# Kernel tuning notes

Measured on AMD Instinct MI355X. Metric: run time of the kernel, lower is better.

## Reference

```python
import jax, jax.numpy as jnp
import numpy as np

B, M, N, D, W = 4, 4096, 4096, 128, 128  # batch/heads, rows, cols, head dim, nnz per row


def setup_inputs() -> dict:
    key = jax.random.key(0)
    kq, kk, kv, kc = jax.random.split(key, 4)
    q3d = jax.random.normal(kq, (B, M, D), dtype=jnp.float32)
    k3d = jax.random.normal(kk, (B, N, D), dtype=jnp.float32)
    v3d = jax.random.normal(kv, (B, N, D), dtype=jnp.float32)
    # CSR with uniform W nonzeros per row: row_offsets = arange(M+1)*W implicitly
    column_indices = jnp.sort(
        jax.random.randint(kc, (M, W), 0, N), axis=-1
    ).astype(jnp.int32)
    return {"q3d": q3d, "k3d": k3d, "v3d": v3d, "column_indices": column_indices}


def reference(q3d, k3d, v3d, column_indices):
    # SDDMM: logits[b, i, j] = q[b, i, :] . k[b, col[i, j], :]  (no 1/sqrt(d) scaling,
    # matching the original module which applies none)
    k_gath = k3d[:, column_indices, :]                     # [B, M, W, D]
    logits = jnp.einsum('bmd,bmwd->bmw', q3d, k_gath)      # [B, M, W]
    # Sparse row-wise softmax over the nonzeros of each row
    weights = jax.nn.softmax(logits, axis=-1)              # [B, M, W]
    # SPMM: out[b, i, :] = sum_j weights[b, i, j] * v[b, col[i, j], :]
    v_gath = v3d[:, column_indices, :]                     # [B, M, W, D]
    out = jnp.einsum('bmw,bmwd->bmd', weights, v_gath)     # [B, M, D]
    return out
```

## Files before the change

kernel.cpp:

```cpp
#include <hip/hip_runtime.h>


typedef __attribute__((ext_vector_type(2))) _Float16 half2v;
typedef __attribute__((ext_vector_type(8))) _Float16 half8;

constexpr int Bc = 4, Mc = 4096, Nc = 4096, Dc = 128, Wc = 128;
constexpr size_t KV_ELEMS = (size_t)Bc * Nc * Dc;
constexpr float EPS_SCREEN = 3e-6f;
constexpr float QS = 127.f / 6.f;
constexpr float INV_S = 1.f / (QS * QS);

__global__ __launch_bounds__(256) void cvt_kernel(
    const float* __restrict__ k3d, _Float16* __restrict__ kh,
    unsigned int* __restrict__ ki8)
{
    const size_t i = ((size_t)blockIdx.x * blockDim.x + threadIdx.x) * 8;
    if (i >= KV_ELEMS) return;
    const float4 ka = *reinterpret_cast<const float4*>(k3d + i);
    const float4 kb = *reinterpret_cast<const float4*>(k3d + i + 4);
    half8 hk;
    hk[0]=(_Float16)ka.x; hk[1]=(_Float16)ka.y; hk[2]=(_Float16)ka.z; hk[3]=(_Float16)ka.w;
    hk[4]=(_Float16)kb.x; hk[5]=(_Float16)kb.y; hk[6]=(_Float16)kb.z; hk[7]=(_Float16)kb.w;
    *reinterpret_cast<half8*>(kh + i) = hk;
    float f[8] = {ka.x, ka.y, ka.z, ka.w, kb.x, kb.y, kb.z, kb.w};
    unsigned int w0 = 0, w1 = 0;
    #pragma unroll
    for (int j = 0; j < 4; ++j) {
        int v = __float2int_rn(f[j] * QS);
        v = max(-127, min(127, v));
        w0 |= ((unsigned int)(v & 0xFF)) << (8 * j);
    }
    #pragma unroll
    for (int j = 0; j < 4; ++j) {
        int v = __float2int_rn(f[4 + j] * QS);
        v = max(-127, min(127, v));
        w1 |= ((unsigned int)(v & 0xFF)) << (8 * j);
    }
    *reinterpret_cast<uint2*>(ki8 + i / 4) = make_uint2(w0, w1);
}

__device__ __forceinline__ float dot8_f16(const half8& qv, const half8& kv) {
    const half2v q0 = {qv[0], qv[1]}, q1 = {qv[2], qv[3]},
                 q2 = {qv[4], qv[5]}, q3 = {qv[6], qv[7]};
    const half2v k0 = {kv[0], kv[1]}, k1 = {kv[2], kv[3]},
                 k2 = {kv[4], kv[5]}, k3 = {kv[6], kv[7]};
    float p = __builtin_amdgcn_fdot2(q0, k0, 0.f, false);
    p = __builtin_amdgcn_fdot2(q1, k1, p, false);
    p = __builtin_amdgcn_fdot2(q2, k2, p, false);
    p = __builtin_amdgcn_fdot2(q3, k3, p, false);
    return p;
}

__global__ __launch_bounds__(64) void sparse_attn_r10(
    const float*        __restrict__ q3d,
    const _Float16*     __restrict__ kh,
    const unsigned int* __restrict__ ki8,
    const float*        __restrict__ v3d,
    const int*          __restrict__ cidx,
    float*              __restrict__ out)
{
    const int blk = blockIdx.x;
    const int xcd = blk & 7;
    const int b   = xcd >> 1;
    const int m   = ((blk >> 3) << 1) | (xcd & 1);
    const int j   = threadIdx.x;

    __shared__ __align__(16) _Float16 qsh[Dc];
    __shared__ __align__(16) unsigned int qpk[Dc / 4];
    __shared__ int   cs[Wc];
    __shared__ int   part[8][Wc + 4];
    __shared__ float rpart[16][17];
    __shared__ int   widx[Wc];
    __shared__ float ls2[Wc];
    __shared__ float wp[Wc];

    {
        const size_t qb = ((size_t)b * Mc + m) * Dc;
        const float qf0 = q3d[qb + j];
        const float qf1 = q3d[qb + 64 + j];
        qsh[j]      = (_Float16)qf0;
        qsh[64 + j] = (_Float16)qf1;
        int v0 = __float2int_rn(qf0 * QS); v0 = max(-127, min(127, v0));
        int v1 = __float2int_rn(qf1 * QS); v1 = max(-127, min(127, v1));
        reinterpret_cast<signed char*>(qpk)[j]      = (signed char)v0;
        reinterpret_cast<signed char*>(qpk)[64 + j] = (signed char)v1;
        cs[j]      = cidx[m * Wc + j];
        cs[64 + j] = cidx[m * Wc + 64 + j];
        widx[j] = 0; widx[64 + j] = 0;
    }
    __syncthreads();

    const int c8 = j & 7;
    const int r8 = j >> 3;
    const uint4* kbq = reinterpret_cast<const uint4*>(ki8 + (size_t)b * Nc * Dc / 4);
    const int qd0 = (int)qpk[c8 * 4 + 0], qd1 = (int)qpk[c8 * 4 + 1],
              qd2 = (int)qpk[c8 * 4 + 2], qd3 = (int)qpk[c8 * 4 + 3];

    int rb[16];
    #pragma unroll
    for (int i = 0; i < 16; ++i) rb[i] = cs[i * 8 + r8] * 8 + c8;
    uint4 kr[16];
    #pragma unroll
    for (int i = 0; i < 16; ++i) kr[i] = kbq[rb[i]];
    #pragma unroll
    for (int i = 0; i < 16; ++i) {
        int d = __builtin_amdgcn_sdot4(qd0, (int)kr[i].x, 0, false);
        d = __builtin_amdgcn_sdot4(qd1, (int)kr[i].y, d, false);
        d = __builtin_amdgcn_sdot4(qd2, (int)kr[i].z, d, false);
        d = __builtin_amdgcn_sdot4(qd3, (int)kr[i].w, d, false);
        part[c8][i * 8 + r8] = d;
    }
    __syncthreads();

    int Li0 = 0, Li1 = 0;
    #pragma unroll
    for (int c = 0; c < 8; ++c) { Li0 += part[c][j]; Li1 += part[c][64 + j]; }
    const float L0 = (float)Li0 * INV_S;
    const float L1 = (float)Li1 * INV_S;

    float mx = fmaxf(L0, L1);
    #pragma unroll
    for (int o = 32; o; o >>= 1) mx = fmaxf(mx, __shfl_xor(mx, o));
    const float e0 = __expf(L0 - mx), e1 = __expf(L1 - mx);
    float ssum = e0 + e1;
    #pragma unroll
    for (int o = 32; o; o >>= 1) ssum += __shfl_xor(ssum, o);
    const float inv_ssum = 1.f / ssum;

    const unsigned long long mk0 = __ballot(e0 * inv_ssum >= EPS_SCREEN);
    const unsigned long long mk1 = __ballot(e1 * inv_ssum >= EPS_SCREEN);
    const int n0 = __popcll(mk0);
    const int n  = n0 + __popcll(mk1);
    const unsigned long long lt = (j == 0) ? 0ull : (~0ull >> (64 - j));
    if (mk0 & (1ull << j)) widx[__popcll(mk0 & lt)]      = cs[j];
    if (mk1 & (1ull << j)) widx[n0 + __popcll(mk1 & lt)] = cs[64 + j];
    __syncthreads();

    const int c16 = j & 15;
    const int r4  = j >> 4;
    const half8*  kb16 = reinterpret_cast<const half8*>(kh + (size_t)b * Nc * Dc);
    const float2* vb2  = reinterpret_cast<const float2*>(v3d + (size_t)b * Nc * Dc);
    const half8 qv = *reinterpret_cast<const half8*>(&qsh[c16 * 8]);

    half8 kk[4];
    #pragma unroll
    for (int v = 0; v < 4; ++v) {
        const int slot = v * 4 + r4;
        kk[v] = (slot < n) ? kb16[widx[slot] * 16 + c16] : half8{};
    }
    float2 vr[16];
    #pragma unroll
    for (int sx = 0; sx < 16; ++sx) {
        vr[sx] = vb2[(size_t)widx[sx] * 64 + j];
    }

    #pragma unroll
    for (int v = 0; v < 4; ++v)
        rpart[v * 4 + r4][c16] = dot8_f16(qv, kk[v]);
    __syncthreads();
    if (j < 16) {
        float sum = 0.f;
        #pragma unroll
        for (int c = 0; c < 16; ++c) sum += rpart[j][c];
        ls2[j] = sum;
    }
    for (int base = 16; base < n; base += 16) {
        __syncthreads();
        #pragma unroll
        for (int v = 0; v < 4; ++v) {
            const int slot = base + v * 4 + r4;
            half8 kx = (slot < n) ? kb16[widx[slot] * 16 + c16] : half8{};
            rpart[v * 4 + r4][c16] = dot8_f16(qv, kx);
        }
        __syncthreads();
        if (j < 16 && base + j < n) {
            float sum = 0.f;
            #pragma unroll
            for (int c = 0; c < 16; ++c) sum += rpart[j][c];
            ls2[base + j] = sum;
        }
    }
    __syncthreads();

    const float A  = (j < n)      ? ls2[j]      : -1e30f;
    const float Bl = (64 + j < n) ? ls2[64 + j] : -1e30f;
    float mx2 = fmaxf(A, Bl);
    #pragma unroll
    for (int o = 32; o; o >>= 1) mx2 = fmaxf(mx2, __shfl_xor(mx2, o));
    const float ea = (j < n)      ? __expf(A - mx2)  : 0.f;
    const float eb = (64 + j < n) ? __expf(Bl - mx2) : 0.f;
    float s2 = ea + eb;
    #pragma unroll
    for (int o = 32; o; o >>= 1) s2 += __shfl_xor(s2, o);
    const float i2 = 1.f / s2;
    if (j < n)      wp[j]      = ea * i2;
    if (64 + j < n) wp[64 + j] = eb * i2;
    __syncthreads();

    float2 acc = {0.f, 0.f};
    #pragma unroll
    for (int sx = 0; sx < 16; ++sx) {
        const float w = (sx < n) ? wp[sx] : 0.f;
        acc.x += w * vr[sx].x;
        acc.y += w * vr[sx].y;
    }
    for (int sx = 16; sx < n; ++sx) {
        const float w = wp[sx];
        const float2 v2 = vb2[(size_t)widx[sx] * 64 + j];
        acc.x += w * v2.x;
        acc.y += w * v2.y;
    }
    reinterpret_cast<float2*>(out + ((size_t)b * Mc + m) * Dc)[j] = acc;
}

extern "C" void kernel_launch(void* const* d_in, const int* in_sizes, int n_in,
                              void* d_out, int out_size, void* d_ws, size_t ws_size,
                              hipStream_t stream) {
    const float* q = (const float*)d_in[0];
    const float* k = (const float*)d_in[1];
    const float* v = (const float*)d_in[2];
    const int*   c = (const int*)d_in[3];
    float*       o = (float*)d_out;
    (void)in_sizes; (void)n_in; (void)out_size; (void)ws_size;

    _Float16*     kh  = (_Float16*)d_ws;
    unsigned int* ki8 = (unsigned int*)((char*)d_ws + KV_ELEMS * sizeof(_Float16));

    const int cvt_threads = 256;
    const int cvt_blocks  = (int)(KV_ELEMS / 8 / cvt_threads);
    cvt_kernel<<<cvt_blocks, cvt_threads, 0, stream>>>(k, kh, ki8);

    sparse_attn_r10<<<dim3(Bc * Mc), dim3(64), 0, stream>>>(q, kh, ki8, v, c, o);
}
```

Baseline: 100.3 us.

## Pack two rows per block with one wave each, using shuffle reductions

Each 128-thread block now processes two query rows, one wave per row, and all block-wide barriers become wave barriers. Partial dot products in both the int8 screening pass and the fp16 rescoring pass are reduced with cross-lane shuffles instead of shared-memory partial arrays. The V accumulation uses float4 loads split across half-waves, combined with a final shuffle. The aim is to remove shared-memory round trips and barrier stalls and to raise occupancy, at the cost of extra shuffle instructions and a different row-to-lane mapping for the screened indices.

```diff
diff --git a/kernel.cpp b/kernel.cpp
--- a/kernel.cpp
+++ b/kernel.cpp
@@ -25,16 +25,16 @@
     float f[8] = {ka.x, ka.y, ka.z, ka.w, kb.x, kb.y, kb.z, kb.w};
     unsigned int w0 = 0, w1 = 0;
     #pragma unroll
-    for (int j = 0; j < 4; ++j) {
-        int v = __float2int_rn(f[j] * QS);
+    for (int jj = 0; jj < 4; ++jj) {
+        int v = __float2int_rn(f[jj] * QS);
         v = max(-127, min(127, v));
-        w0 |= ((unsigned int)(v & 0xFF)) << (8 * j);
-    }
-    #pragma unroll
-    for (int j = 0; j < 4; ++j) {
-        int v = __float2int_rn(f[4 + j] * QS);
+        w0 |= ((unsigned int)(v & 0xFF)) << (8 * jj);
+    }
+    #pragma unroll
+    for (int jj = 0; jj < 4; ++jj) {
+        int v = __float2int_rn(f[4 + jj] * QS);
         v = max(-127, min(127, v));
-        w1 |= ((unsigned int)(v & 0xFF)) << (8 * j);
+        w1 |= ((unsigned int)(v & 0xFF)) << (8 * jj);
     }
     *reinterpret_cast<uint2*>(ki8 + i / 4) = make_uint2(w0, w1);
 }
@@ -51,7 +51,7 @@
     return p;
 }
 
-__global__ __launch_bounds__(64) void sparse_attn_r10(
+__global__ __launch_bounds__(128, 8) void sparse_attn_r11(
     const float*        __restrict__ q3d,
     const _Float16*     __restrict__ kh,
     const unsigned int* __restrict__ ki8,
@@ -60,61 +60,66 @@
     float*              __restrict__ out)
 {
     const int blk = blockIdx.x;
+    const int u   = threadIdx.x >> 6;
+    const int j   = threadIdx.x & 63;
     const int xcd = blk & 7;
     const int b   = xcd >> 1;
-    const int m   = ((blk >> 3) << 1) | (xcd & 1);
-    const int j   = threadIdx.x;
-
-    __shared__ __align__(16) _Float16 qsh[Dc];
-    __shared__ __align__(16) unsigned int qpk[Dc / 4];
-    __shared__ int   cs[Wc];
-    __shared__ int   part[8][Wc + 4];
-    __shared__ float rpart[16][17];
-    __shared__ int   widx[Wc];
-    __shared__ float ls2[Wc];
-    __shared__ float wp[Wc];
+    const int m   = ((blk >> 3) << 2) | ((xcd & 1) << 1) | u;
+
+    __shared__ __align__(16) _Float16 qsh[2][Dc];
+    __shared__ unsigned int qpk[2][Dc / 4];
+    __shared__ int   cs[2][Wc];
+    __shared__ int   widx[2][Wc];
+    __shared__ float ls2[2][Wc];
+    __shared__ float wp[2][Wc];
 
     {
         const size_t qb = ((size_t)b * Mc + m) * Dc;
         const float qf0 = q3d[qb + j];
         const float qf1 = q3d[qb + 64 + j];
-        qsh[j]      = (_Float16)qf0;
-        qsh[64 + j] = (_Float16)qf1;
+        qsh[u][j]      = (_Float16)qf0;
+        qsh[u][64 + j] = (_Float16)qf1;
         int v0 = __float2int_rn(qf0 * QS); v0 = max(-127, min(127, v0));
         int v1 = __float2int_rn(qf1 * QS); v1 = max(-127, min(127, v1));
-        reinterpret_cast<signed char*>(qpk)[j]      = (signed char)v0;
-        reinterpret_cast<signed char*>(qpk)[64 + j] = (signed char)v1;
-        cs[j]      = cidx[m * Wc + j];
-        cs[64 + j] = cidx[m * Wc + 64 + j];
-        widx[j] = 0; widx[64 + j] = 0;
-    }
-    __syncthreads();
+        reinterpret_cast<signed char*>(qpk[u])[j]      = (signed char)v0;
+        reinterpret_cast<signed char*>(qpk[u])[64 + j] = (signed char)v1;
+        cs[u][j]      = cidx[m * Wc + j];
+        cs[u][64 + j] = cidx[m * Wc + 64 + j];
+        widx[u][j] = 0; widx[u][64 + j] = 0;
+        wp[u][j] = 0.f;  wp[u][64 + j] = 0.f;
+    }
+    __builtin_amdgcn_wave_barrier();
 
     const int c8 = j & 7;
     const int r8 = j >> 3;
     const uint4* kbq = reinterpret_cast<const uint4*>(ki8 + (size_t)b * Nc * Dc / 4);
-    const int qd0 = (int)qpk[c8 * 4 + 0], qd1 = (int)qpk[c8 * 4 + 1],
-              qd2 = (int)qpk[c8 * 4 + 2], qd3 = (int)qpk[c8 * 4 + 3];
-
-    int rb[16];
-    #pragma unroll
-    for (int i = 0; i < 16; ++i) rb[i] = cs[i * 8 + r8] * 8 + c8;
-    uint4 kr[16];
-    #pragma unroll
-    for (int i = 0; i < 16; ++i) kr[i] = kbq[rb[i]];
-    #pragma unroll
-    for (int i = 0; i < 16; ++i) {
-        int d = __builtin_amdgcn_sdot4(qd0, (int)kr[i].x, 0, false);
-        d = __builtin_amdgcn_sdot4(qd1, (int)kr[i].y, d, false);
-        d = __builtin_amdgcn_sdot4(qd2, (int)kr[i].z, d, false);
-        d = __builtin_amdgcn_sdot4(qd3, (int)kr[i].w, d, false);
-        part[c8][i * 8 + r8] = d;
-    }
-    __syncthreads();
+    const int qd0 = (int)qpk[u][c8 * 4 + 0], qd1 = (int)qpk[u][c8 * 4 + 1],
+              qd2 = (int)qpk[u][c8 * 4 + 2], qd3 = (int)qpk[u][c8 * 4 + 3];
 
     int Li0 = 0, Li1 = 0;
     #pragma unroll
-    for (int c = 0; c < 8; ++c) { Li0 += part[c][j]; Li1 += part[c][64 + j]; }
+    for (int bt = 0; bt < 4; ++bt) {
+        int rw[4];
+        #pragma unroll
+        for (int ii = 0; ii < 4; ++ii)
+            rw[ii] = cs[u][(bt * 4 + ii) * 8 + r8] * 8 + c8;
+        uint4 kr[4];
+        #pragma unroll
+        for (int ii = 0; ii < 4; ++ii) kr[ii] = kbq[rw[ii]];
+        #pragma unroll
+        for (int ii = 0; ii < 4; ++ii) {
+            const int i = bt * 4 + ii;
+            int d = __builtin_amdgcn_sdot4(qd0, (int)kr[ii].x, 0, false);
+            d = __builtin_amdgcn_sdot4(qd1, (int)kr[ii].y, d, false);
+            d = __builtin_amdgcn_sdot4(qd2, (int)kr[ii].z, d, false);
+            d = __builtin_amdgcn_sdot4(qd3, (int)kr[ii].w, d, false);
+            d += __shfl_xor(d, 1);
+            d += __shfl_xor(d, 2);
+            d += __shfl_xor(d, 4);
+            if (i == c8)     Li0 = d;
+            if (i == 8 + c8) Li1 = d;
+        }
+    }
     const float L0 = (float)Li0 * INV_S;
     const float L1 = (float)Li1 * INV_S;
 
@@ -132,85 +137,78 @@
     const int n0 = __popcll(mk0);
     const int n  = n0 + __popcll(mk1);
     const unsigned long long lt = (j == 0) ? 0ull : (~0ull >> (64 - j));
-    if (mk0 & (1ull << j)) widx[__popcll(mk0 & lt)]      = cs[j];
-    if (mk1 & (1ull << j)) widx[n0 + __popcll(mk1 & lt)] = cs[64 + j];
-    __syncthreads();
-
-    const int c16 = j & 15;
-    const int r4  = j >> 4;
-    const half8*  kb16 = reinterpret_cast<const half8*>(kh + (size_t)b * Nc * Dc);
-    const float2* vb2  = reinterpret_cast<const float2*>(v3d + (size_t)b * Nc * Dc);
-    const half8 qv = *reinterpret_cast<const half8*>(&qsh[c16 * 8]);
-
-    half8 kk[4];
+    const int w0r = c8 * 8 + r8;
+    if (mk0 & (1ull << j)) widx[u][__popcll(mk0 & lt)]      = cs[u][w0r];
+    if (mk1 & (1ull << j)) widx[u][n0 + __popcll(mk1 & lt)] = cs[u][64 + w0r];
+    __builtin_amdgcn_wave_barrier();
+
+    const int c16 = j & 15, r4 = j >> 4;
+    const half8* kb16 = reinterpret_cast<const half8*>(kh + (size_t)b * Nc * Dc);
+    const half8 qv = *reinterpret_cast<const half8*>(&qsh[u][c16 * 8]);
     #pragma unroll
     for (int v = 0; v < 4; ++v) {
         const int slot = v * 4 + r4;
-        kk[v] = (slot < n) ? kb16[widx[slot] * 16 + c16] : half8{};
-    }
-    float2 vr[16];
-    #pragma unroll
-    for (int sx = 0; sx < 16; ++sx) {
-        vr[sx] = vb2[(size_t)widx[sx] * 64 + j];
-    }
-
-    #pragma unroll
-    for (int v = 0; v < 4; ++v)
-        rpart[v * 4 + r4][c16] = dot8_f16(qv, kk[v]);
-    __syncthreads();
-    if (j < 16) {
-        float sum = 0.f;
-        #pragma unroll
-        for (int c = 0; c < 16; ++c) sum += rpart[j][c];
-        ls2[j] = sum;
+        const half8 kk = kb16[widx[u][slot] * 16 + c16];
+        float pp = dot8_f16(qv, kk);
+        pp += __shfl_xor(pp, 1);
+        pp += __shfl_xor(pp, 2);
+        pp += __shfl_xor(pp, 4);
+        pp += __shfl_xor(pp, 8);
+        if (c16 == v) ls2[u][slot] = pp;
     }
     for (int base = 16; base < n; base += 16) {
-        __syncthreads();
         #pragma unroll
         for (int v = 0; v < 4; ++v) {
             const int slot = base + v * 4 + r4;
-            half8 kx = (slot < n) ? kb16[widx[slot] * 16 + c16] : half8{};
-            rpart[v * 4 + r4][c16] = dot8_f16(qv, kx);
+            const half8 kk = kb16[widx[u][slot] * 16 + c16];
+            float pp = dot8_f16(qv, kk);
+            pp += __shfl_xor(pp, 1);
+            pp += __shfl_xor(pp, 2);
+            pp += __shfl_xor(pp, 4);
+            pp += __shfl_xor(pp, 8);
+            if (c16 == v) ls2[u][slot] = pp;
         }
-        __syncthreads();
-        if (j < 16 && base + j < n) {
-            float sum = 0.f;
-            #pragma unroll
-            for (int c = 0; c < 16; ++c) sum += rpart[j][c];
-            ls2[base + j] = sum;
-        }
-    }
-    __syncthreads();
-
-    const float A  = (j < n)      ? ls2[j]      : -1e30f;
-    const float Bl = (64 + j < n) ? ls2[64 + j] : -1e30f;
-    float mx2 = fmaxf(A, Bl);
+    }
+    __builtin_amdgcn_wave_barrier();
+
+    const float A  = (j < n)      ? ls2[u][j]      : -1e30f;
+    const float B2 = (64 + j < n) ? ls2[u][64 + j] : -1e30f;
+    float mx2 = fmaxf(A, B2);
     #pragma unroll
     for (int o = 32; o; o >>= 1) mx2 = fmaxf(mx2, __shfl_xor(mx2, o));
     const float ea = (j < n)      ? __expf(A - mx2)  : 0.f;
-    const float eb = (64 + j < n) ? __expf(Bl - mx2) : 0.f;
+    const float eb = (64 + j < n) ? __expf(B2 - mx2) : 0.f;
     float s2 = ea + eb;
     #pragma unroll
     for (int o = 32; o; o >>= 1) s2 += __shfl_xor(s2, o);
     const float i2 = 1.f / s2;
-    if (j < n)      wp[j]      = ea * i2;
-    if (64 + j < n) wp[64 + j] = eb * i2;
-    __syncthreads();
-
-    float2 acc = {0.f, 0.f};
-    #pragma unroll
-    for (int sx = 0; sx < 16; ++sx) {
-        const float w = (sx < n) ? wp[sx] : 0.f;
-        acc.x += w * vr[sx].x;
-        acc.y += w * vr[sx].y;
-    }
-    for (int sx = 16; sx < n; ++sx) {
-        const float w = wp[sx];
-        const float2 v2 = vb2[(size_t)widx[sx] * 64 + j];
-        acc.x += w * v2.x;
-        acc.y += w * v2.y;
-    }
-    reinterpret_cast<float2*>(out + ((size_t)b * Mc + m) * Dc)[j] = acc;
+    if (j < n)      wp[u][j]      = ea * i2;
+    if (64 + j < n) wp[u][64 + j] = eb * i2;
+    __builtin_amdgcn_wave_barrier();
+
+    const int h = j >> 5, c32 = j & 31;
+    const float4* vb4 = reinterpret_cast<const float4*>(v3d + (size_t)b * Nc * Dc);
+    float4 acc = {0.f, 0.f, 0.f, 0.f};
+    #pragma unroll
+    for (int i = 0; i < 8; ++i) {
+        const int slot = 2 * i + h;
+        const float w = wp[u][slot];
+        const float4 v4 = vb4[(size_t)widx[u][slot] * 32 + c32];
+        acc.x += w * v4.x; acc.y += w * v4.y;
+        acc.z += w * v4.z; acc.w += w * v4.w;
+    }
+    for (int slot = 16 + h; slot < n; slot += 2) {
+        const float w = wp[u][slot];
+        const float4 v4 = vb4[(size_t)widx[u][slot] * 32 + c32];
+        acc.x += w * v4.x; acc.y += w * v4.y;
+        acc.z += w * v4.z; acc.w += w * v4.w;
+    }
+    acc.x += __shfl_xor(acc.x, 32);
+    acc.y += __shfl_xor(acc.y, 32);
+    acc.z += __shfl_xor(acc.z, 32);
+    acc.w += __shfl_xor(acc.w, 32);
+    if (j < 32)
+        reinterpret_cast<float4*>(out + ((size_t)b * Mc + m) * Dc)[j] = acc;
 }
 
 extern "C" void kernel_launch(void* const* d_in, const int* in_sizes, int n_in,
@@ -230,5 +228,5 @@
     const int cvt_blocks  = (int)(KV_ELEMS / 8 / cvt_threads);
     cvt_kernel<<<cvt_blocks, cvt_threads, 0, stream>>>(k, kh, ki8);
 
-    sparse_attn_r10<<<dim3(Bc * Mc), dim3(64), 0, stream>>>(q, kh, ki8, v, c, o);
-}
+    sparse_attn_r11<<<dim3(Bc * Mc / 2), dim3(128), 0, stream>>>(q, kh, ki8, v, c, o);
+}
```

After: 105.0 us. 4.6% more time.

## Pack four rows per block with per-wave shared buffers and wave-level barriers

Applied to the files above, without the earlier changes.

The attention kernel now runs 256-thread blocks where each of four waves handles its own query row, with per-wave shared memory slices. Block-wide __syncthreads are replaced by wave barriers, since each wave only shares data with itself. The int8 screening pass splits its 16 gathered K loads into two halves of 8, with the second half loaded while the first is reduced, which lowers register pressure. The aim is to cut block-scheduling and barrier overhead and raise occupancy, at the cost of larger per-block LDS and reliance on intra-wave ordering of LDS accesses.

```diff
diff --git a/kernel.cpp b/kernel.cpp
--- a/kernel.cpp
+++ b/kernel.cpp
@@ -25,16 +25,16 @@
     float f[8] = {ka.x, ka.y, ka.z, ka.w, kb.x, kb.y, kb.z, kb.w};
     unsigned int w0 = 0, w1 = 0;
     #pragma unroll
-    for (int j = 0; j < 4; ++j) {
-        int v = __float2int_rn(f[j] * QS);
+    for (int jj = 0; jj < 4; ++jj) {
+        int v = __float2int_rn(f[jj] * QS);
         v = max(-127, min(127, v));
-        w0 |= ((unsigned int)(v & 0xFF)) << (8 * j);
-    }
-    #pragma unroll
-    for (int j = 0; j < 4; ++j) {
-        int v = __float2int_rn(f[4 + j] * QS);
+        w0 |= ((unsigned int)(v & 0xFF)) << (8 * jj);
+    }
+    #pragma unroll
+    for (int jj = 0; jj < 4; ++jj) {
+        int v = __float2int_rn(f[4 + jj] * QS);
         v = max(-127, min(127, v));
-        w1 |= ((unsigned int)(v & 0xFF)) << (8 * j);
+        w1 |= ((unsigned int)(v & 0xFF)) << (8 * jj);
     }
     *reinterpret_cast<uint2*>(ki8 + i / 4) = make_uint2(w0, w1);
 }
@@ -51,7 +51,7 @@
     return p;
 }
 
-__global__ __launch_bounds__(64) void sparse_attn_r10(
+__global__ __launch_bounds__(256, 6) void sparse_attn_r12(
     const float*        __restrict__ q3d,
     const _Float16*     __restrict__ kh,
     const unsigned int* __restrict__ ki8,
@@ -60,61 +60,78 @@
     float*              __restrict__ out)
 {
     const int blk = blockIdx.x;
+    const int u   = threadIdx.x >> 6;
+    const int j   = threadIdx.x & 63;
     const int xcd = blk & 7;
     const int b   = xcd >> 1;
-    const int m   = ((blk >> 3) << 1) | (xcd & 1);
-    const int j   = threadIdx.x;
-
-    __shared__ __align__(16) _Float16 qsh[Dc];
-    __shared__ __align__(16) unsigned int qpk[Dc / 4];
-    __shared__ int   cs[Wc];
-    __shared__ int   part[8][Wc + 4];
-    __shared__ float rpart[16][17];
-    __shared__ int   widx[Wc];
-    __shared__ float ls2[Wc];
-    __shared__ float wp[Wc];
+    const int m   = ((blk >> 3) << 3) | ((xcd & 1) << 2) | u;
+
+    __shared__ __align__(16) _Float16 qsh[4][Dc];
+    __shared__ unsigned int qpk[4][Dc / 4];
+    __shared__ int   cs[4][Wc];
+    __shared__ int   part[4][8][66];
+    __shared__ float rpart[4][16][17];
+    __shared__ int   widx[4][Wc];
+    __shared__ float ls2[4][Wc];
+    __shared__ float wp[4][Wc];
 
     {
         const size_t qb = ((size_t)b * Mc + m) * Dc;
         const float qf0 = q3d[qb + j];
         const float qf1 = q3d[qb + 64 + j];
-        qsh[j]      = (_Float16)qf0;
-        qsh[64 + j] = (_Float16)qf1;
+        qsh[u][j]      = (_Float16)qf0;
+        qsh[u][64 + j] = (_Float16)qf1;
         int v0 = __float2int_rn(qf0 * QS); v0 = max(-127, min(127, v0));
         int v1 = __float2int_rn(qf1 * QS); v1 = max(-127, min(127, v1));
-        reinterpret_cast<signed char*>(qpk)[j]      = (signed char)v0;
-        reinterpret_cast<signed char*>(qpk)[64 + j] = (signed char)v1;
-        cs[j]      = cidx[m * Wc + j];
-        cs[64 + j] = cidx[m * Wc + 64 + j];
-        widx[j] = 0; widx[64 + j] = 0;
-    }
-    __syncthreads();
+        reinterpret_cast<signed char*>(qpk[u])[j]      = (signed char)v0;
+        reinterpret_cast<signed char*>(qpk[u])[64 + j] = (signed char)v1;
+        cs[u][j]      = cidx[m * Wc + j];
+        cs[u][64 + j] = cidx[m * Wc + 64 + j];
+        widx[u][j] = 0; widx[u][64 + j] = 0;
+        wp[u][j] = 0.f;  wp[u][64 + j] = 0.f;
+    }
+    __builtin_amdgcn_wave_barrier();
 
     const int c8 = j & 7;
     const int r8 = j >> 3;
     const uint4* kbq = reinterpret_cast<const uint4*>(ki8 + (size_t)b * Nc * Dc / 4);
-    const int qd0 = (int)qpk[c8 * 4 + 0], qd1 = (int)qpk[c8 * 4 + 1],
-              qd2 = (int)qpk[c8 * 4 + 2], qd3 = (int)qpk[c8 * 4 + 3];
-
-    int rb[16];
-    #pragma unroll
-    for (int i = 0; i < 16; ++i) rb[i] = cs[i * 8 + r8] * 8 + c8;
-    uint4 kr[16];
-    #pragma unroll
-    for (int i = 0; i < 16; ++i) kr[i] = kbq[rb[i]];
-    #pragma unroll
-    for (int i = 0; i < 16; ++i) {
+    const int qd0 = (int)qpk[u][c8 * 4 + 0], qd1 = (int)qpk[u][c8 * 4 + 1],
+              qd2 = (int)qpk[u][c8 * 4 + 2], qd3 = (int)qpk[u][c8 * 4 + 3];
+
+    int rbAll[16];
+    #pragma unroll
+    for (int i = 0; i < 16; ++i) rbAll[i] = cs[u][i * 8 + r8] * 8 + c8;
+
+    uint4 kr[8];
+    #pragma unroll
+    for (int i = 0; i < 8; ++i) kr[i] = kbq[rbAll[i]];
+    #pragma unroll
+    for (int i = 0; i < 8; ++i) {
         int d = __builtin_amdgcn_sdot4(qd0, (int)kr[i].x, 0, false);
         d = __builtin_amdgcn_sdot4(qd1, (int)kr[i].y, d, false);
         d = __builtin_amdgcn_sdot4(qd2, (int)kr[i].z, d, false);
         d = __builtin_amdgcn_sdot4(qd3, (int)kr[i].w, d, false);
-        part[c8][i * 8 + r8] = d;
-    }
-    __syncthreads();
-
-    int Li0 = 0, Li1 = 0;
-    #pragma unroll
-    for (int c = 0; c < 8; ++c) { Li0 += part[c][j]; Li1 += part[c][64 + j]; }
+        part[u][c8][i * 8 + r8] = d;
+    }
+    uint4 kr2[8];
+    #pragma unroll
+    for (int i = 0; i < 8; ++i) kr2[i] = kbq[rbAll[8 + i]];
+
+    int Li0 = 0;
+    #pragma unroll
+    for (int c = 0; c < 8; ++c) Li0 += part[u][c][j];
+    __builtin_amdgcn_wave_barrier();
+    #pragma unroll
+    for (int i = 0; i < 8; ++i) {
+        int d = __builtin_amdgcn_sdot4(qd0, (int)kr2[i].x, 0, false);
+        d = __builtin_amdgcn_sdot4(qd1, (int)kr2[i].y, d, false);
+        d = __builtin_amdgcn_sdot4(qd2, (int)kr2[i].z, d, false);
+        d = __builtin_amdgcn_sdot4(qd3, (int)kr2[i].w, d, false);
+        part[u][c8][i * 8 + r8] = d;
+    }
+    int Li1 = 0;
+    #pragma unroll
+    for (int c = 0; c < 8; ++c) Li1 += part[u][c][j];
     const float L0 = (float)Li0 * INV_S;
     const float L1 = (float)Li1 * INV_S;
 
@@ -132,81 +149,81 @@
     const int n0 = __popcll(mk0);
     const int n  = n0 + __popcll(mk1);
     const unsigned long long lt = (j == 0) ? 0ull : (~0ull >> (64 - j));
-    if (mk0 & (1ull << j)) widx[__popcll(mk0 & lt)]      = cs[j];
-    if (mk1 & (1ull << j)) widx[n0 + __popcll(mk1 & lt)] = cs[64 + j];
-    __syncthreads();
+    if (mk0 & (1ull << j)) widx[u][__popcll(mk0 & lt)]      = cs[u][j];
+    if (mk1 & (1ull << j)) widx[u][n0 + __popcll(mk1 & lt)] = cs[u][64 + j];
+    __builtin_amdgcn_wave_barrier();
 
     const int c16 = j & 15;
     const int r4  = j >> 4;
     const half8*  kb16 = reinterpret_cast<const half8*>(kh + (size_t)b * Nc * Dc);
     const float2* vb2  = reinterpret_cast<const float2*>(v3d + (size_t)b * Nc * Dc);
-    const half8 qv = *reinterpret_cast<const half8*>(&qsh[c16 * 8]);
+    const half8 qv = *reinterpret_cast<const half8*>(&qsh[u][c16 * 8]);
 
     half8 kk[4];
     #pragma unroll
     for (int v = 0; v < 4; ++v) {
         const int slot = v * 4 + r4;
-        kk[v] = (slot < n) ? kb16[widx[slot] * 16 + c16] : half8{};
+        kk[v] = (slot < n) ? kb16[widx[u][slot] * 16 + c16] : half8{};
     }
     float2 vr[16];
     #pragma unroll
     for (int sx = 0; sx < 16; ++sx) {
-        vr[sx] = vb2[(size_t)widx[sx] * 64 + j];
+        vr[sx] = vb2[(size_t)widx[u][sx] * 64 + j];
     }
 
     #pragma unroll
     for (int v = 0; v < 4; ++v)
-        rpart[v * 4 + r4][c16] = dot8_f16(qv, kk[v]);
-    __syncthreads();
+        rpart[u][v * 4 + r4][c16] = dot8_f16(qv, kk[v]);
+    __builtin_amdgcn_wave_barrier();
     if (j < 16) {
         float sum = 0.f;
         #pragma unroll
-        for (int c = 0; c < 16; ++c) sum += rpart[j][c];
-        ls2[j] = sum;
+        for (int c = 0; c < 16; ++c) sum += rpart[u][j][c];
+        ls2[u][j] = sum;
     }
     for (int base = 16; base < n; base += 16) {
-        __syncthreads();
+        __builtin_amdgcn_wave_barrier();
         #pragma unroll
         for (int v = 0; v < 4; ++v) {
             const int slot = base + v * 4 + r4;
-            half8 kx = (slot < n) ? kb16[widx[slot] * 16 + c16] : half8{};
-            rpart[v * 4 + r4][c16] = dot8_f16(qv, kx);
+            half8 kx = (slot < n) ? kb16[widx[u][slot] * 16 + c16] : half8{};
+            rpart[u][v * 4 + r4][c16] = dot8_f16(qv, kx);
         }
-        __syncthreads();
+        __builtin_amdgcn_wave_barrier();
         if (j < 16 && base + j < n) {
             float sum = 0.f;
             #pragma unroll
-            for (int c = 0; c < 16; ++c) sum += rpart[j][c];
-            ls2[base + j] = sum;
+            for (int c = 0; c < 16; ++c) sum += rpart[u][j][c];
+            ls2[u][base + j] = sum;
         }
     }
-    __syncthreads();
-
-    const float A  = (j < n)      ? ls2[j]      : -1e30f;
-    const float Bl = (64 + j < n) ? ls2[64 + j] : -1e30f;
-    float mx2 = fmaxf(A, Bl);
+    __builtin_amdgcn_wave_barrier();
+
+    const float A  = (j < n)      ? ls2[u][j]      : -1e30f;
+    const float B2 = (64 + j < n) ? ls2[u][64 + j] : -1e30f;
+    float mx2 = fmaxf(A, B2);
     #pragma unroll
     for (int o = 32; o; o >>= 1) mx2 = fmaxf(mx2, __shfl_xor(mx2, o));
     const float ea = (j < n)      ? __expf(A - mx2)  : 0.f;
-    const float eb = (64 + j < n) ? __expf(Bl - mx2) : 0.f;
+    const float eb = (64 + j < n) ? __expf(B2 - mx2) : 0.f;
     float s2 = ea + eb;
     #pragma unroll
     for (int o = 32; o; o >>= 1) s2 += __shfl_xor(s2, o);
     const float i2 = 1.f / s2;
-    if (j < n)      wp[j]      = ea * i2;
-    if (64 + j < n) wp[64 + j] = eb * i2;
-    __syncthreads();
+    if (j < n)      wp[u][j]      = ea * i2;
+    if (64 + j < n) wp[u][64 + j] = eb * i2;
+    __builtin_amdgcn_wave_barrier();
 
     float2 acc = {0.f, 0.f};
     #pragma unroll
     for (int sx = 0; sx < 16; ++sx) {
-        const float w = (sx < n) ? wp[sx] : 0.f;
+        const float w = (sx < n) ? wp[u][sx] : 0.f;
         acc.x += w * vr[sx].x;
         acc.y += w * vr[sx].y;
     }
     for (int sx = 16; sx < n; ++sx) {
-        const float w = wp[sx];
-        const float2 v2 = vb2[(size_t)widx[sx] * 64 + j];
+        const float w = wp[u][sx];
+        const float2 v2 = vb2[(size_t)widx[u][sx] * 64 + j];
         acc.x += w * v2.x;
         acc.y += w * v2.y;
     }
@@ -230,5 +247,5 @@
     const int cvt_blocks  = (int)(KV_ELEMS / 8 / cvt_threads);
     cvt_kernel<<<cvt_blocks, cvt_threads, 0, stream>>>(k, kh, ki8);
 
-    sparse_attn_r10<<<dim3(Bc * Mc), dim3(64), 0, stream>>>(q, kh, ki8, v, c, o);
-}
+    sparse_attn_r12<<<dim3(Bc * Mc / 4), dim3(256), 0, stream>>>(q, kh, ki8, v, c, o);
+}
```

New measurement: 109.1 us. +8.7%, slower.
